# Performance work log

Hardware: AMD Instinct MI355X
Metric: run time of the kernel (lower is better)

## Reference

```python
import jax, jax.numpy as jnp
import numpy as np

B, L, D, H = 4, 1024, 256, 8
TEMP = float(np.sqrt(D))
EPS_SM = 1e-6
EPS_LN = 1e-5


def setup_inputs() -> dict:
    key = jax.random.key(0)
    ks = jax.random.split(key, 8)
    std = float(np.sqrt(2.0 / (D * 2)))
    return {
        "q": jax.random.normal(ks[0], (B, L, D), jnp.float32),
        "mask": jax.random.randint(ks[1], (B, L, L), 0, 2, jnp.int32),
        "k": jax.random.normal(ks[2], (B, L, D), jnp.float32),
        "v": jax.random.normal(ks[3], (B, L, D), jnp.float32),
        "w_qs": jax.random.normal(ks[4], (H * D, D), jnp.float32) * std,
        "w_ks": jax.random.normal(ks[5], (H * D, D), jnp.float32) * std,
        "w_vs": jax.random.normal(ks[6], (H * D, D), jnp.float32) * std,
        "fc_w": jax.random.normal(ks[7], (D, H * D), jnp.float32) * float(np.sqrt(2.0 / (D + H * D))),
        "fc_b": jnp.zeros((D,), jnp.float32),
        "ln_g": jnp.ones((D,), jnp.float32),
        "ln_b": jnp.zeros((D,), jnp.float32),
    }


def masked_softmax(x, m):
    # repo's layers.masked_softmax: clamp, mask-mul, stable exp, mask-mul, normalize
    x = jnp.clip(x, -15.0, 15.0) * m
    e = jnp.exp(x - jnp.max(x, axis=-1, keepdims=True)) * m
    return e / (jnp.sum(e, axis=-1, keepdims=True) + EPS_SM)


def reference(q, mask, k, v, w_qs, w_ks, w_vs, fc_w, fc_b, ln_g, ln_b):
    residual = q
    m = mask.astype(q.dtype)[:, None, :, :]          # [B,1,Lq,Lk]
    # projections to per-head full-dim: [B,L,H,D]
    qh = (q @ w_qs.T).reshape(B, L, H, D)
    kh = (k @ w_ks.T).reshape(B, L, H, D)
    vh = (v @ w_vs.T).reshape(B, L, H, D)
    scores = jnp.einsum("bqhd,bkhd->bhqk", qh, kh) / TEMP   # [B,H,Lq,Lk]
    attn = masked_softmax(scores, m)
    out = jnp.einsum("bhqk,bkhd->bqhd", attn, vh).reshape(B, L, H * D)
    out = out @ fc_w.T + fc_b                         # [B,L,D]
    out = out + residual
    mu = jnp.mean(out, axis=-1, keepdims=True)
    var = jnp.var(out, axis=-1, keepdims=True)
    out = (out - mu) / jnp.sqrt(var + EPS_LN) * ln_g + ln_b
    # match torch attn layout: [H*B, Lq, Lk] (head-major)
    attn_hb = jnp.transpose(attn, (1, 0, 2, 3)).reshape(H * B, L, L)
    return out, attn_hb
```

## Files before the change

### kernel.cpp

```cpp
#include <hip/hip_runtime.h>
#include <cstdint>
#include <math.h>

#define Bsz 4
#define Lsz 1024
#define Dsz 256
#define Hsz 8
#define HD  2048
#define NROWS (Bsz*Lsz)
#define INV_TEMP 0.0625f

typedef __attribute__((ext_vector_type(8))) short bf16x8;
typedef __attribute__((ext_vector_type(4))) float f32x4;

__device__ inline unsigned short f2bf(float f) {
    union { float f; unsigned u; } x; x.f = f;
    unsigned r = x.u + 0x7fffu + ((x.u >> 16) & 1u);
    return (unsigned short)(r >> 16);
}
__device__ inline float bf2f(unsigned short u) {
    union { unsigned u; float f; } x; x.u = (unsigned)u << 16; return x.f;
}

#define GBL(p) ((const __attribute__((address_space(1))) unsigned int*)(p))
#define LDS(p) ((__attribute__((address_space(3))) unsigned int*)(p))

template<int N> __device__ __forceinline__ void vmw() {
    if constexpr (N == 0)       asm volatile("s_waitcnt vmcnt(0)"  ::: "memory");
    else if constexpr (N == 4)  asm volatile("s_waitcnt vmcnt(4)"  ::: "memory");
    else if constexpr (N == 6)  asm volatile("s_waitcnt vmcnt(6)"  ::: "memory");
    else if constexpr (N == 10) asm volatile("s_waitcnt vmcnt(10)" ::: "memory");
    else if constexpr (N == 14) asm volatile("s_waitcnt vmcnt(14)" ::: "memory");
    else static_assert(N == 0, "unsupported vmcnt literal");
}

template <int TMv, int TNv, typename OutT, int EPI, int MINW, bool FUSE,
          int GX, int GY, int GZ>
__global__ __launch_bounds__(256, MINW) void gemm_bt(
    const unsigned short* __restrict__ A, const unsigned short* __restrict__ Bm,
    OutT* __restrict__ C,
    int K, int lda, int ldb, int ldc, int inner,
    long long sA1, long long sA2, long long sB1, long long sB2,
    long long sC1, long long sC2, float alpha,
    const unsigned char* __restrict__ maskb, long long sM2,
    const float* __restrict__ invs, long long sI1, long long sI2,
    float* __restrict__ aux,
    const unsigned short* __restrict__ A2, const unsigned short* __restrict__ B2,
    unsigned short* __restrict__ C2)
{
    constexpr int WMv = TMv / 2, WNv = TNv / 2;
    constexpr int IT = TMv / 32, JT = TNv / 32;
    constexpr int APASS = TMv / 32, NPASS = (TMv + TNv) / 32;
    constexpr int TILE = (TMv + TNv) * 64;
    constexpr int G = GX * GY * GZ;
    static_assert(G % 8 == 0, "bijective XCD swizzle needs G%8==0");
    static_assert(NPASS == 6 || NPASS == 10, "vmcnt literals assume NPASS in {6,10}");

    const int lid = blockIdx.x + GX * (blockIdx.y + GY * blockIdx.z);
    const int nid = (lid & 7) * (G >> 3) + (lid >> 3);
    int mx = nid % GX;
    const int t1g = nid / GX;
    int my = t1g % GY;
    const int z  = t1g / GY;

    if constexpr (FUSE) {
        if (z >= 2) {
            const int idx = my * 64 + mx;
            if (idx >= 256) return;
            mx = idx & 31; my = idx >> 5;
            const int b = z - 2;
            A   = A2;
            Bm  = B2 + (size_t)b * ((size_t)Lsz * Dsz);
            C   = (OutT*)(C2 + (size_t)b * ((size_t)HD * Lsz));
            ldc = Lsz;
        } else {
            A  += (size_t)z * sA2;
            Bm += (size_t)z * sB2;
            C  += (size_t)z * sC2;
        }
    } else {
        const int i1 = z / inner;
        const int i2 = z % inner;
        A  += (size_t)i1 * sA1 + (size_t)i2 * sA2;
        Bm += (size_t)i1 * sB1 + (size_t)i2 * sB2;
        C  += (size_t)i1 * sC1 + (size_t)i2 * sC2;
        if (EPI == 1) { maskb += (size_t)i2 * sM2; aux += (size_t)z * Lsz; }
        if (EPI == 2) { invs  += (size_t)i1 * sI1 + (size_t)i2 * sI2; aux += (size_t)z * Lsz * Lsz; }
    }

    __shared__ unsigned short S[2 * TILE];

    const int t    = threadIdx.x;
    const int lane = t & 63;
    const int w    = t >> 6;
    const int wm   = w & 1;
    const int wn   = w >> 1;
    const int m0   = mx * TMv;
    const int n0   = my * TNv;

    const int rA = t >> 3;
    const int ch = ((t & 7) ^ (rA & 7)) * 8;
    const unsigned short* gA = A  + (size_t)(m0 + rA) * lda + ch;
    const unsigned short* gB = Bm + (size_t)(n0 + rA) * ldb + ch;

    const int fr = lane & 15;
    const int q  = lane >> 4;

    f32x4 acc[IT][JT];
#pragma unroll
    for (int i = 0; i < IT; ++i)
#pragma unroll
        for (int j = 0; j < JT; ++j) acc[i][j] = (f32x4){0.f, 0.f, 0.f, 0.f};

    auto stage = [&](unsigned short* Sb, int k0) {
#pragma unroll
        for (int p = 0; p < NPASS; ++p) {
            const unsigned short* src = (p < APASS)
                ? (gA + (size_t)p * 32 * lda + k0)
                : (gB + (size_t)(p - APASS) * 32 * ldb + k0);
            __builtin_amdgcn_global_load_lds(GBL(src), LDS(Sb + p * 2048 + t * 8), 16, 0, 0);
        }
    };
    auto kstep = [&](const unsigned short* As) {
        const unsigned short* Bs = As + TMv * 64;
#pragma unroll
        for (int ks = 0; ks < 2; ++ks) {
            const int slot = ((ks * 4 + q) ^ (fr & 7)) * 8;
            bf16x8 a[IT], b[JT];
#pragma unroll
            for (int i = 0; i < IT; ++i)
                a[i] = *(const bf16x8*)(As + (wm * WMv + i * 16 + fr) * 64 + slot);
#pragma unroll
            for (int j = 0; j < JT; ++j)
                b[j] = *(const bf16x8*)(Bs + (wn * WNv + j * 16 + fr) * 64 + slot);
#pragma unroll
            for (int i = 0; i < IT; ++i)
#pragma unroll
                for (int j = 0; j < JT; ++j)
                    acc[i][j] = __builtin_amdgcn_mfma_f32_16x16x32_bf16(a[i], b[j], acc[i][j], 0, 0, 0);
        }
    };

    const int nk = K >> 6;

    float ainv[EPI == 2 ? (TMv / 32) : 1];
    if constexpr (EPI == 2) {
        const int rsub = lane >> 3;
#pragma unroll
        for (int pass = 0; pass < TMv / 32; ++pass)
            ainv[pass] = 1.0f / (invs[m0 + w * (TMv / 4) + pass * 8 + rsub] + 1e-6f);
        vmw<0>();
    }

    stage(S, 0);

    for (int kt = 0; kt < nk; ++kt) {
        if (kt + 1 < nk) stage(S + ((kt + 1) & 1) * TILE, (kt + 1) << 6);

        if constexpr (EPI == 2) {
            if (kt + 1 < nk) { if (kt >= 1) vmw<NPASS + 4>(); else vmw<NPASS>(); }
            else             { if (kt >= 1) vmw<4>();         else vmw<0>(); }
        } else {
            if (kt + 1 < nk) vmw<NPASS>(); else vmw<0>();
        }
        __builtin_amdgcn_s_barrier();

        kstep(S + (kt & 1) * TILE);

        if constexpr (EPI == 2) {
            const unsigned short* As = S + (kt & 1) * TILE;
            const int chunk = lane & 7;
            const int rsub  = lane >> 3;
#pragma unroll
            for (int pass = 0; pass < TMv / 32; ++pass) {
                const int row = w * (TMv / 4) + pass * 8 + rsub;
                const uint4 u = *(const uint4*)(As + row * 64 + ((chunk ^ (row & 7)) * 8));
                const float iv = ainv[pass];
                float4 lo, hi;
                lo.x = bf2f((unsigned short)(u.x & 0xffff)) * iv; lo.y = bf2f((unsigned short)(u.x >> 16)) * iv;
                lo.z = bf2f((unsigned short)(u.y & 0xffff)) * iv; lo.w = bf2f((unsigned short)(u.y >> 16)) * iv;
                hi.x = bf2f((unsigned short)(u.z & 0xffff)) * iv; hi.y = bf2f((unsigned short)(u.z >> 16)) * iv;
                hi.z = bf2f((unsigned short)(u.w & 0xffff)) * iv; hi.w = bf2f((unsigned short)(u.w >> 16)) * iv;
                float* op = aux + (size_t)(m0 + row) * Lsz + (kt << 6) + chunk * 8;
                *(float4*)op = lo;
                *(float4*)(op + 4) = hi;
            }
        }

        asm volatile("s_waitcnt lgkmcnt(0)" ::: "memory");
        __builtin_amdgcn_s_barrier();
    }

    float einv[EPI == 2 ? IT : 1][EPI == 2 ? 4 : 1];
    if constexpr (EPI == 2) {
#pragma unroll
        for (int i = 0; i < IT; ++i)
#pragma unroll
            for (int r = 0; r < 4; ++r)
                einv[i][r] = 1.0f / (invs[m0 + wm * WMv + i * 16 + q * 4 + r] + 1e-6f);
    }

#pragma unroll
    for (int i = 0; i < IT; ++i) {
#pragma unroll
        for (int r = 0; r < 4; ++r) {
            const int row = m0 + wm * WMv + i * 16 + q * 4 + r;
            float rsum = 0.f;
#pragma unroll
            for (int j = 0; j < JT; ++j) {
                const int col = n0 + wn * WNv + j * 16 + fr;
                float vv = acc[i][j][r] * alpha;
                if (EPI == 0) {
                    if constexpr (sizeof(OutT) == 4)
                        C[(size_t)row * ldc + col] = (OutT)vv;
                    else
                        ((unsigned short*)C)[(size_t)row * ldc + col] = f2bf(vv);
                } else if (EPI == 1) {
                    const float m = (float)maskb[(size_t)row * Lsz + col];
                    vv = fminf(fmaxf(vv, -15.f), 15.f) * m;
                    vv = __expf(vv) * m;
                    const unsigned short us = f2bf(vv);
                    ((unsigned short*)C)[(size_t)row * ldc + col] = us;
                    rsum += bf2f(us);
                } else {
                    vv *= einv[i][r];
                    ((unsigned short*)C)[(size_t)row * ldc + col] = f2bf(vv);
                }
            }
            if constexpr (EPI == 1) {
#pragma unroll
                for (int o = 1; o <= 8; o <<= 1) rsum += __shfl_xor(rsum, o, 64);
                if (fr == 0) atomicAdd(&aux[row], rsum);
            }
        }
    }
}

__global__ __launch_bounds__(256) void cast_all(
    const float* __restrict__ q, const float* __restrict__ k, const float* __restrict__ v,
    const float* __restrict__ wq, const float* __restrict__ wk, const float* __restrict__ wv,
    const float* __restrict__ fw, const int* __restrict__ mask,
    unsigned short* __restrict__ qb, unsigned short* __restrict__ kb, unsigned short* __restrict__ vb,
    unsigned short* __restrict__ wqb, unsigned short* __restrict__ wkb, unsigned short* __restrict__ wvb,
    unsigned short* __restrict__ fwb, unsigned char* __restrict__ mb,
    float* __restrict__ rs)
{
    const int gid = blockIdx.x * 256 + threadIdx.x;
    const int NQ = 262144;
    const int NW = 131072;
    const int NF = 3 * NQ + 4 * NW;
    const int NM = 1048576;
    if (gid >= NF) {
        const int off = gid - NF;
        if (off >= NM) {
            const int ri = off - NM;
            if (ri < 8192) ((float4*)rs)[ri] = (float4){0.f, 0.f, 0.f, 0.f};
            return;
        }
        const int4 mi = ((const int4*)mask)[off];
        uchar4 o;
        o.x = mi.x ? 1 : 0;
        o.y = mi.y ? 1 : 0;
        o.z = mi.z ? 1 : 0;
        o.w = mi.w ? 1 : 0;
        ((uchar4*)mb)[off] = o;
        return;
    }
    const float* src; unsigned short* dst; int off;
    if      (gid < NQ)            { src = q;  dst = qb;  off = gid; }
    else if (gid < 2 * NQ)        { src = k;  dst = kb;  off = gid - NQ; }
    else if (gid < 3 * NQ)        { src = v;  dst = vb;  off = gid - 2 * NQ; }
    else if (gid < 3 * NQ + NW)   { src = wq; dst = wqb; off = gid - 3 * NQ; }
    else if (gid < 3 * NQ + 2*NW) { src = wk; dst = wkb; off = gid - 3 * NQ - NW; }
    else if (gid < 3 * NQ + 3*NW) { src = wv; dst = wvb; off = gid - 3 * NQ - 2 * NW; }
    else                          { src = fw; dst = fwb; off = gid - 3 * NQ - 3 * NW; }
    float4 f = ((const float4*)src)[off];
    ushort4 o;
    o.x = f2bf(f.x); o.y = f2bf(f.y); o.z = f2bf(f.z); o.w = f2bf(f.w);
    ((ushort4*)dst)[off] = o;
}

__global__ __launch_bounds__(256) void ln_kernel(const float* __restrict__ gout,
                                                 const float* __restrict__ qin,
                                                 const float* __restrict__ fc_b,
                                                 const float* __restrict__ ln_g,
                                                 const float* __restrict__ ln_b,
                                                 float* __restrict__ out)
{
    const int row = blockIdx.x;
    const int t = threadIdx.x;
    const size_t idx = (size_t)row * Dsz + t;
    const size_t P = (size_t)NROWS * Dsz;
    const float val = gout[idx] + gout[idx + P] + gout[idx + 2 * P] + gout[idx + 3 * P]
                    + fc_b[t] + qin[idx];

    __shared__ float red[4];
    float s = val;
#pragma unroll
    for (int o = 32; o > 0; o >>= 1) s += __shfl_down(s, o, 64);
    const int lane = t & 63, w = t >> 6;
    if (lane == 0) red[w] = s;
    __syncthreads();
    const float mu = (red[0] + red[1] + red[2] + red[3]) * (1.0f / Dsz);
    __syncthreads();

    float d = val - mu;
    float s2 = d * d;
#pragma unroll
    for (int o = 32; o > 0; o >>= 1) s2 += __shfl_down(s2, o, 64);
    if (lane == 0) red[w] = s2;
    __syncthreads();
    const float var = (red[0] + red[1] + red[2] + red[3]) * (1.0f / Dsz);

    out[idx] = d * rsqrtf(var + 1e-5f) * ln_g[t] + ln_b[t];
}

extern "C" void kernel_launch(void* const* d_in, const int* in_sizes, int n_in,
                              void* d_out, int out_size, void* d_ws, size_t ws_size,
                              hipStream_t stream)
{
    const float* q    = (const float*)d_in[0];
    const int*   mask = (const int*)d_in[1];
    const float* k    = (const float*)d_in[2];
    const float* v    = (const float*)d_in[3];
    const float* w_qs = (const float*)d_in[4];
    const float* w_ks = (const float*)d_in[5];
    const float* w_vs = (const float*)d_in[6];
    const float* fc_w = (const float*)d_in[7];
    const float* fc_b = (const float*)d_in[8];
    const float* ln_g = (const float*)d_in[9];
    const float* ln_b = (const float*)d_in[10];

    float* out  = (float*)d_out;
    float* attn = (float*)d_out + (size_t)NROWS * Dsz;

    unsigned short* wsu = (unsigned short*)d_ws;
    unsigned short* qh     = wsu;
    unsigned short* kh     = qh + (size_t)NROWS * HD;
    unsigned short* q_bf   = kh + (size_t)NROWS * HD;
    unsigned short* k_bf   = q_bf + (size_t)NROWS * Dsz;
    unsigned short* v_bf   = k_bf + (size_t)NROWS * Dsz;
    unsigned short* wq_bf  = v_bf + (size_t)NROWS * Dsz;
    unsigned short* wk_bf  = wq_bf + (size_t)HD * Dsz;
    unsigned short* wv_bf  = wk_bf + (size_t)HD * Dsz;
    unsigned short* vt     = wv_bf + (size_t)HD * Dsz;
    unsigned short* attn_e = vt + (size_t)Bsz * HD * Lsz;
    unsigned short* attnv  = attn_e + (size_t)32 * Lsz * Lsz;
    unsigned short* fcw_bf = attnv + (size_t)NROWS * HD;
    float*          rowsum = (float*)(fcw_bf + (size_t)Dsz * HD);
    float*          fcout  = rowsum + 32768;
    unsigned char*  maskb  = (unsigned char*)(fcout + (size_t)4 * NROWS * Dsz);

    dim3 blk(256);

    cast_all<<<dim3(9248), blk, 0, stream>>>(q, k, v, w_qs, w_ks, w_vs, fc_w, mask,
                                             q_bf, k_bf, v_bf, wq_bf, wk_bf, wv_bf, fcw_bf, maskb,
                                             rowsum);

    {
        dim3 grid(NROWS / 64, HD / 128, 6);
        gemm_bt<64, 128, unsigned short, 0, 3, true, 64, 16, 6><<<grid, blk, 0, stream>>>(
            q_bf, wq_bf, qh,
            Dsz, Dsz, Dsz, HD, 2,
            0, (long long)NROWS * Dsz, 0, (long long)HD * Dsz, 0, (long long)NROWS * HD,
            1.0f, nullptr, 0, nullptr, 0, 0, nullptr,
            wv_bf, v_bf, vt);
    }

    {
        dim3 grid(Lsz / 64, Lsz / 128, Hsz * Bsz);
        gemm_bt<64, 128, unsigned short, 1, 3, false, 16, 8, 32><<<grid, blk, 0, stream>>>(
            qh, kh, attn_e,
            Dsz, HD, HD, Lsz, Bsz,
            Dsz, (long long)Lsz * HD, Dsz, (long long)Lsz * HD,
            (long long)Bsz * Lsz * Lsz, (long long)Lsz * Lsz,
            INV_TEMP, maskb, (long long)Lsz * Lsz, nullptr, 0, 0, rowsum,
            nullptr, nullptr, nullptr);
    }

    {
        dim3 grid(Lsz / 64, 1, Hsz * Bsz);
        gemm_bt<64, 256, unsigned short, 2, 2, false, 16, 1, 32><<<grid, blk, 0, stream>>>(
            attn_e, vt, attnv,
            Lsz, Lsz, Lsz, HD, Bsz,
            (long long)Bsz * Lsz * Lsz, (long long)Lsz * Lsz,
            (long long)Dsz * Lsz, (long long)HD * Lsz,
            Dsz, (long long)Lsz * HD,
            1.0f, nullptr, 0, rowsum, (long long)Bsz * Lsz, (long long)Lsz, attn,
            nullptr, nullptr, nullptr);
    }

    {
        dim3 grid(NROWS / 64, Dsz / 128, 4);
        gemm_bt<64, 128, float, 0, 3, false, 64, 2, 4><<<grid, blk, 0, stream>>>(
            attnv, fcw_bf, fcout,
            512, HD, HD, Dsz, 4,
            0, 512, 0, 512, 0, (long long)NROWS * Dsz,
            1.0f, nullptr, 0, nullptr, 0, 0, nullptr,
            nullptr, nullptr, nullptr);
    }

    ln_kernel<<<dim3(NROWS), blk, 0, stream>>>(fcout, q, fc_b, ln_g, ln_b, out);
}
```

Before: 328.0 us.

## Stage GEMM epilogue through LDS for coalesced vectorized global stores

Accumulator tiles are first written to shared memory as fp32 with a padded stride. Threads then reread them row-contiguously, so each thread handles a 32-column segment and issues 16-byte vector stores and mask loads instead of scattered 2-byte stores. The masked-exp, rowsum and normalization epilogues are moved to this new layout, and the rowsum reduction now uses fewer shuffles and atomics. The cost is an extra LDS round trip and a barrier, and the static asserts tie the design to TNv=128 and to the LDS size. An unused variable z is also introduced.

```diff
diff --git a/kernel.cpp b/kernel.cpp
--- a/kernel.cpp
+++ b/kernel.cpp
@@ -55,38 +55,43 @@
     constexpr int G = GX * GY * GZ;
     static_assert(G % 8 == 0, "bijective XCD swizzle needs G%8==0");
     static_assert(NPASS == 6 || NPASS == 10, "vmcnt literals assume NPASS in {6,10}");
+    static_assert(EPI != 1 || TNv == 128, "EPI=1 rowsum shfl assumes 4 segs");
+    static_assert(TMv * (TNv + 4) * 4 <= 2 * TILE * 2, "epilogue LDS overflow");
+
+    const int z  = blockIdx.z;
 
     const int lid = blockIdx.x + GX * (blockIdx.y + GY * blockIdx.z);
     const int nid = (lid & 7) * (G >> 3) + (lid >> 3);
     int mx = nid % GX;
     const int t1g = nid / GX;
     int my = t1g % GY;
-    const int z  = t1g / GY;
+    const int zz = t1g / GY;
 
     if constexpr (FUSE) {
-        if (z >= 2) {
+        if (zz >= 2) {
             const int idx = my * 64 + mx;
             if (idx >= 256) return;
             mx = idx & 31; my = idx >> 5;
-            const int b = z - 2;
+            const int b = zz - 2;
             A   = A2;
             Bm  = B2 + (size_t)b * ((size_t)Lsz * Dsz);
             C   = (OutT*)(C2 + (size_t)b * ((size_t)HD * Lsz));
             ldc = Lsz;
         } else {
-            A  += (size_t)z * sA2;
-            Bm += (size_t)z * sB2;
-            C  += (size_t)z * sC2;
+            A  += (size_t)zz * sA2;
+            Bm += (size_t)zz * sB2;
+            C  += (size_t)zz * sC2;
         }
     } else {
-        const int i1 = z / inner;
-        const int i2 = z % inner;
+        const int i1 = zz / inner;
+        const int i2 = zz % inner;
         A  += (size_t)i1 * sA1 + (size_t)i2 * sA2;
         Bm += (size_t)i1 * sB1 + (size_t)i2 * sB2;
         C  += (size_t)i1 * sC1 + (size_t)i2 * sC2;
-        if (EPI == 1) { maskb += (size_t)i2 * sM2; aux += (size_t)z * Lsz; }
-        if (EPI == 2) { invs  += (size_t)i1 * sI1 + (size_t)i2 * sI2; aux += (size_t)z * Lsz * Lsz; }
-    }
+        if (EPI == 1) { maskb += (size_t)i2 * sM2; aux += (size_t)zz * Lsz; }
+        if (EPI == 2) { invs  += (size_t)i1 * sI1 + (size_t)i2 * sI2; aux += (size_t)zz * Lsz * Lsz; }
+    }
+    (void)z;
 
     __shared__ unsigned short S[2 * TILE];
 
@@ -191,46 +196,78 @@
         __builtin_amdgcn_s_barrier();
     }
 
-    float einv[EPI == 2 ? IT : 1][EPI == 2 ? 4 : 1];
-    if constexpr (EPI == 2) {
+    {
+        float* Lf = (float*)S;
+        constexpr int LP = TNv + 4;
 #pragma unroll
         for (int i = 0; i < IT; ++i)
 #pragma unroll
-            for (int r = 0; r < 4; ++r)
-                einv[i][r] = 1.0f / (invs[m0 + wm * WMv + i * 16 + q * 4 + r] + 1e-6f);
-    }
-
-#pragma unroll
-    for (int i = 0; i < IT; ++i) {
-#pragma unroll
-        for (int r = 0; r < 4; ++r) {
-            const int row = m0 + wm * WMv + i * 16 + q * 4 + r;
-            float rsum = 0.f;
-#pragma unroll
             for (int j = 0; j < JT; ++j) {
-                const int col = n0 + wn * WNv + j * 16 + fr;
-                float vv = acc[i][j][r] * alpha;
-                if (EPI == 0) {
-                    if constexpr (sizeof(OutT) == 4)
-                        C[(size_t)row * ldc + col] = (OutT)vv;
-                    else
-                        ((unsigned short*)C)[(size_t)row * ldc + col] = f2bf(vv);
-                } else if (EPI == 1) {
-                    const float m = (float)maskb[(size_t)row * Lsz + col];
-                    vv = fminf(fmaxf(vv, -15.f), 15.f) * m;
-                    vv = __expf(vv) * m;
-                    const unsigned short us = f2bf(vv);
-                    ((unsigned short*)C)[(size_t)row * ldc + col] = us;
-                    rsum += bf2f(us);
-                } else {
-                    vv *= einv[i][r];
-                    ((unsigned short*)C)[(size_t)row * ldc + col] = f2bf(vv);
+                const int col = wn * WNv + j * 16 + fr;
+#pragma unroll
+                for (int r = 0; r < 4; ++r) {
+                    const int row = wm * WMv + i * 16 + q * 4 + r;
+                    Lf[row * LP + col] = acc[i][j][r] * alpha;
                 }
             }
-            if constexpr (EPI == 1) {
-#pragma unroll
-                for (int o = 1; o <= 8; o <<= 1) rsum += __shfl_xor(rsum, o, 64);
-                if (fr == 0) atomicAdd(&aux[row], rsum);
+        __syncthreads();
+
+        constexpr int SEGS = TNv / 32;
+        constexpr int RPI  = 256 / SEGS;
+#pragma unroll
+        for (int it2 = 0; it2 < TMv / RPI; ++it2) {
+            const int row = it2 * RPI + t / SEGS;
+            const int c0  = (t % SEGS) * 32;
+            const float* src = Lf + row * LP + c0;
+
+            if constexpr (EPI == 0 && sizeof(OutT) == 4) {
+                float* dst = (float*)C + (size_t)(m0 + row) * ldc + n0 + c0;
+#pragma unroll
+                for (int v4 = 0; v4 < 8; ++v4)
+                    *(f32x4*)(dst + v4 * 4) = *(const f32x4*)(src + v4 * 4);
+            } else if constexpr (EPI == 0) {
+                unsigned short* dst = (unsigned short*)C + (size_t)(m0 + row) * ldc + n0 + c0;
+#pragma unroll
+                for (int v8 = 0; v8 < 4; ++v8) {
+                    bf16x8 o;
+#pragma unroll
+                    for (int e = 0; e < 8; ++e) o[e] = (short)f2bf(src[v8 * 8 + e]);
+                    *(bf16x8*)(dst + v8 * 8) = o;
+                }
+            } else if constexpr (EPI == 1) {
+                unsigned short* dst = (unsigned short*)C + (size_t)(m0 + row) * ldc + n0 + c0;
+                const unsigned char* mrow = maskb + (size_t)(m0 + row) * Lsz + n0 + c0;
+                unsigned char mloc[32];
+                *(uint4*)mloc        = *(const uint4*)mrow;
+                *(uint4*)(mloc + 16) = *(const uint4*)(mrow + 16);
+                float rsum = 0.f;
+#pragma unroll
+                for (int v8 = 0; v8 < 4; ++v8) {
+                    bf16x8 o;
+#pragma unroll
+                    for (int e = 0; e < 8; ++e) {
+                        const float m = (float)mloc[v8 * 8 + e];
+                        float vv = fminf(fmaxf(src[v8 * 8 + e], -15.f), 15.f) * m;
+                        vv = __expf(vv) * m;
+                        const unsigned short us = f2bf(vv);
+                        o[e] = (short)us;
+                        rsum += bf2f(us);
+                    }
+                    *(bf16x8*)(dst + v8 * 8) = o;
+                }
+                rsum += __shfl_xor(rsum, 1, 64);
+                rsum += __shfl_xor(rsum, 2, 64);
+                if ((t & 3) == 0) atomicAdd(&aux[m0 + row], rsum);
+            } else {
+                unsigned short* dst = (unsigned short*)C + (size_t)(m0 + row) * ldc + n0 + c0;
+                const float iv = 1.0f / (invs[m0 + row] + 1e-6f);
+#pragma unroll
+                for (int v8 = 0; v8 < 4; ++v8) {
+                    bf16x8 o;
+#pragma unroll
+                    for (int e = 0; e < 8; ++e) o[e] = (short)f2bf(src[v8 * 8 + e] * iv);
+                    *(bf16x8*)(dst + v8 * 8) = o;
+                }
             }
         }
     }
```

Result: no change. 326.2 us (-0.6%).
